# Kernel optimization log

Hardware: AMD Instinct MI355X
Metric: run time of the kernel (lower is better)

Reference implementation:

```python
import jax, jax.numpy as jnp
import numpy as np

B, S, D = 8, 2048, 2048  # seq_len must equal dim for this module's math to type-check


def setup_inputs() -> dict:
    key = jax.random.key(0)
    ks = jax.random.split(key, 9)
    sc = 1.0 / np.sqrt(D)
    return {
        "query": jax.random.normal(ks[0], (B, S, D), jnp.float32),
        "key_": jax.random.normal(ks[1], (B, S, D), jnp.float32),
        "value": jax.random.normal(ks[2], (B, S, D), jnp.float32),
        "Wq": jax.random.normal(ks[3], (D, D), jnp.float32) * sc,
        "bq": jax.random.normal(ks[4], (D,), jnp.float32) * 0.01,
        "Wk": jax.random.normal(ks[5], (D, D), jnp.float32) * sc,
        "bk": jax.random.normal(ks[6], (D,), jnp.float32) * 0.01,
        "Wv": jax.random.normal(ks[7], (D, D), jnp.float32) * sc,
        "bv": jax.random.normal(ks[8], (D,), jnp.float32) * 0.01,
    }


def reference(query, key_, value, Wq, bq, Wk, bk, Wv, bv):
    scale_factor = 1.0  # forward default
    # Linear projections (torch Linear: x @ W^T + b)
    q = jnp.einsum('bsd,ed->bse', query, Wq) + bq   # [B,S,D]
    k = jnp.einsum('bsd,ed->bse', key_, Wk) + bk    # [B,S,D]
    v = jnp.einsum('bsd,ed->bse', value, Wv) + bv   # [B,S,D]
    # Transpose last two dims, then matmul: [B,D,S] @ [B,D,S] (valid since S == D)
    qT = jnp.swapaxes(q, -2, -1)
    kT = jnp.swapaxes(k, -2, -1)
    qk = jnp.matmul(qT, kT) * scale_factor          # [B,D,S]
    attn = jax.nn.softmax(qk, axis=-1)
    # dropout_p = 0 -> identity
    out = jnp.matmul(attn, v)                       # [B,D,D]
    return jnp.swapaxes(out, -2, -1)
```

## Files before the change

kernel.cpp:

```cpp
#include <hip/hip_runtime.h>
#include <hip/hip_fp16.h>


using half8_t = __attribute__((ext_vector_type(8))) _Float16;
using f32x4   = __attribute__((ext_vector_type(4))) float;

static constexpr int NB = 8;
static constexpr int Sd = 2048;
static constexpr long MAT = (long)Sd * Sd;

__device__ __forceinline__ void gload16(const _Float16* g, _Float16* l) {
  __builtin_amdgcn_global_load_lds(
      (const __attribute__((address_space(1))) void*)g,
      (__attribute__((address_space(3))) void*)l, 16, 0, 0);
}
__device__ __forceinline__ void barrier_() { asm volatile("s_barrier" ::: "memory"); }
#define VMCNT(n) asm volatile("s_waitcnt vmcnt(" #n ")" ::: "memory")
#define SCHEDB() __builtin_amdgcn_sched_barrier(0)

template<bool SPLIT>
__global__ __launch_bounds__(256) void presplit(const float* __restrict__ in,
    _Float16* __restrict__ h, _Float16* __restrict__ l, long n8, float scl)
{
  long i = (long)blockIdx.x * 256 + threadIdx.x;
  const long stride = (long)gridDim.x * 256;
  for (; i < n8; i += stride) {
    const f32x4* p = (const f32x4*)(in + i * 8);
    f32x4 a = p[0], b = p[1];
    half8_t hh, ll;
#pragma unroll
    for (int j = 0; j < 4; j++) {
      float x = a[j] * scl; _Float16 hv = (_Float16)x;
      hh[j] = hv; if constexpr (SPLIT) ll[j] = (_Float16)(x - (float)hv);
      float y = b[j] * scl; _Float16 hw = (_Float16)y;
      hh[4 + j] = hw; if constexpr (SPLIT) ll[4 + j] = (_Float16)(y - (float)hw);
    }
    *(half8_t*)(h + i * 8) = hh;
    if constexpr (SPLIT) *(half8_t*)(l + i * 8) = ll;
  }
}

template<int NSEG, int BIAS, int OUT>
__global__ __launch_bounds__(512, 2) void gemm10(
    const _Float16* __restrict__ Ah, const _Float16* __restrict__ Al, long sA,
    const _Float16* __restrict__ Bh, long sB,
    const float* __restrict__ bias, float cscale,
    void* __restrict__ Cp, void* __restrict__ Clp, long sC)
{
  constexpr int NT = NSEG * 32;
  __shared__ __align__(16) _Float16 LA[4][8192];
  __shared__ __align__(16) _Float16 LB[4][8192];

  const int t = threadIdx.x, w = t >> 6, l = t & 63;

  const int wg = blockIdx.x;
  const int swz = (wg & 7) * 64 + (wg >> 3);
  const int bz = swz >> 6, rem = swz & 63;
  const int by = rem >> 3, bx = rem & 7;

  const _Float16* PAh = Ah + (size_t)bz * sA + (size_t)(by * 256) * Sd;
  const _Float16* PBh = Bh + (size_t)bz * sB + (size_t)(bx * 256) * Sd;
  const _Float16* PAl = (NSEG == 2)
      ? Al + (size_t)bz * sA + (size_t)(by * 256) * Sd : PAh;

  const int s7 = t & 7;
  const int lkS = (s7 >> 1) ^ ((t >> 3) & 3);
  const size_t srcoff = (size_t)(2 * (t >> 3) + (s7 & 1)) * Sd + lkS * 8;
  const int du0 = w * 512;

  const int wm = (w >> 2) * 128, wn = (w & 3) * 64;
  const int lm = l & 15, lkr = l >> 4;
  const int sprime = ((lkr ^ ((lm >> 1) & 3)) << 1) | (lm & 1);
  const int aoff = (wm >> 1) * 128 + (lm >> 1) * 128 + sprime * 16;
  const int boff = (wn >> 1) * 128 + (lm >> 1) * 128 + sprime * 16;

  auto srcA = [&](int hp) -> const _Float16* {
    if constexpr (NSEG == 2) return (hp >> 6) ? PAl : PAh;
    return PAh;
  };
  auto koOf = [&](int hp) -> int {
    if constexpr (NSEG == 2) return (hp & 63) * 32;
    return hp * 32;
  };
  auto stageH = [&](int hp) {
    const int u = hp & 3;
    const _Float16* a = srcA(hp) + koOf(hp);
    const _Float16* b = PBh + koOf(hp);
    gload16(a + srcoff, LA[u] + du0);
    gload16(a + srcoff + (size_t)128 * Sd, LA[u] + du0 + 4096);
    gload16(b + srcoff, LB[u] + du0);
    gload16(b + srcoff + (size_t)128 * Sd, LB[u] + du0 + 4096);
  };

  f32x4 acc[8][4] = {};
  half8_t fA0[8], fB0[4], fA1[8], fB1[4];

  auto readF = [&](int u, half8_t (&fa)[8], half8_t (&fb)[4]) {
#pragma unroll
    for (int f = 0; f < 8; f++)
      fa[f] = *(const half8_t*)((const char*)LA[u] + aoff + f * 1024);
#pragma unroll
    for (int n = 0; n < 4; n++)
      fb[n] = *(const half8_t*)((const char*)LB[u] + boff + n * 1024);
  };
  auto mfma32 = [&](const half8_t (&fa)[8], const half8_t (&fb)[4]) {
    __builtin_amdgcn_s_setprio(1);
#pragma unroll
    for (int f = 0; f < 8; f++)
#pragma unroll
      for (int n = 0; n < 4; n++)
        acc[f][n] = __builtin_amdgcn_mfma_f32_16x16x32_f16(fa[f], fb[n], acc[f][n], 0, 0, 0);
    __builtin_amdgcn_s_setprio(0);
  };

  stageH(0); stageH(1); stageH(2);
  VMCNT(4);
  barrier_();
  readF(0, fA0, fB0);

  for (int j = 0; j < NT - 1; ++j) {
    const int p0 = 2 * j;
    readF((p0 + 1) & 3, fA1, fB1);
    stageH(p0 + 3);
    SCHEDB();
    mfma32(fA0, fB0);
    VMCNT(4);
    barrier_();
    readF((p0 + 2) & 3, fA0, fB0);
    if (j < NT - 2) stageH(p0 + 4);
    SCHEDB();
    mfma32(fA1, fB1);
    if (j == NT - 2) { VMCNT(0); } else { VMCNT(4); }
    barrier_();
  }
  {
    const int p0 = 2 * (NT - 1);
    readF((p0 + 1) & 3, fA1, fB1);
    SCHEDB();
    mfma32(fA0, fB0);
    SCHEDB();
    mfma32(fA1, fB1);
  }

  const int row_base = by * 256 + wm + (lkr << 2);
  const int col_base = bx * 256 + wn + lm;
#pragma unroll
  for (int fm = 0; fm < 8; fm++)
#pragma unroll
    for (int fn = 0; fn < 4; fn++) {
      const int n = col_base + fn * 16;
      float bcol = 0.f;
      if constexpr (BIAS == 1) bcol = bias[n];
#pragma unroll
      for (int r = 0; r < 4; r++) {
        const int m = row_base + fm * 16 + r;
        float v = acc[fm][fn][r] * cscale;
        if constexpr (BIAS == 1) v += bcol;
        if constexpr (BIAS == 2) v += bias[m];
        const size_t ci = (size_t)bz * sC + (size_t)m * Sd + n;
        if constexpr (OUT == 0) ((float*)Cp)[ci] = v;
        else if constexpr (OUT == 1) ((_Float16*)Cp)[ci] = (_Float16)v;
        else if constexpr (OUT == 3) ((_Float16*)Cp)[ci] = (_Float16)(v * 16.0f);
        else {
          float sv = v * 16.0f;
          _Float16 hv = (_Float16)sv;
          ((_Float16*)Cp)[ci]  = hv;
          ((_Float16*)Clp)[ci] = (_Float16)(sv - (float)hv);
        }
      }
    }
}

__global__ __launch_bounds__(256) void softmax_rows(const float* __restrict__ X,
                                                    _Float16* __restrict__ P)
{
  __shared__ float red[4];
  const size_t row = blockIdx.x;
  const float* x = X + row * Sd;
  _Float16* p = P + row * Sd;
  const int t = threadIdx.x;
  float v[8];
  float mx = -1e30f;
#pragma unroll
  for (int i = 0; i < 8; i++) { v[i] = x[t + 256 * i]; mx = fmaxf(mx, v[i]); }
#pragma unroll
  for (int o = 32; o > 0; o >>= 1) mx = fmaxf(mx, __shfl_xor(mx, o, 64));
  if ((t & 63) == 0) red[t >> 6] = mx;
  __syncthreads();
  mx = fmaxf(fmaxf(red[0], red[1]), fmaxf(red[2], red[3]));
  __syncthreads();
  float s = 0.f;
#pragma unroll
  for (int i = 0; i < 8; i++) { v[i] = __expf(v[i] - mx); s += v[i]; }
#pragma unroll
  for (int o = 32; o > 0; o >>= 1) s += __shfl_xor(s, o, 64);
  if ((t & 63) == 0) red[t >> 6] = s;
  __syncthreads();
  s = red[0] + red[1] + red[2] + red[3];
  float inv = 1.f / s;
#pragma unroll
  for (int i = 0; i < 8; i++) p[t + 256 * i] = (_Float16)(v[i] * inv);
}

extern "C" void kernel_launch(void* const* d_in, const int* in_sizes, int n_in,
                              void* d_out, int out_size, void* d_ws, size_t ws_size,
                              hipStream_t stream)
{
  const float* query = (const float*)d_in[0];
  const float* key_  = (const float*)d_in[1];
  const float* value = (const float*)d_in[2];
  const float* Wq = (const float*)d_in[3];
  const float* bq = (const float*)d_in[4];
  const float* Wk = (const float*)d_in[5];
  const float* bk = (const float*)d_in[6];
  const float* Wv = (const float*)d_in[7];
  const float* bv = (const float*)d_in[8];

  char* ws = (char*)d_ws;
  char* ob = (char*)d_out;
  const size_t M64 = (size_t)NB * MAT * 2;

  _Float16* q_h  = (_Float16*)(ws);
  _Float16* k_h  = (_Float16*)(ws);
  _Float16* k_l  = (_Float16*)(ws + M64);
  float*    qk   = (float*)(ws);
  _Float16* qT_h = (_Float16*)(ws + 2 * M64);
  _Float16* qT_l = (_Float16*)(ws + 3 * M64);
  _Float16* P    = qT_h;
  _Float16* vT   = qT_l;
  _Float16* kk_h = (_Float16*)(ws + 4 * M64);
  _Float16* val_h = (_Float16*)(ws + 5 * M64);

  _Float16* wq_h = (_Float16*)(ob);
  _Float16* wq_l = (_Float16*)(ob + (MAT * 2));
  _Float16* wk_h = (_Float16*)(ob + 2 * (MAT * 2));
  _Float16* wv_h = (_Float16*)(ob + 3 * (MAT * 2));
  float* out = (float*)d_out;

  dim3 blk256(256), blk512(512);
  dim3 gg(512);
  const long NQ8 = (long)NB * MAT / 8;
  const long NW8 = MAT / 8;

  presplit<false><<<dim3(2048), blk256, 0, stream>>>(query, q_h, nullptr, NQ8, 16.f);
  presplit<true><<<dim3(2048), blk256, 0, stream>>>(Wq, wq_h, wq_l, NW8, 16.f);
  gemm10<2, 2, 2><<<gg, blk512, 0, stream>>>(wq_h, wq_l, 0, q_h, MAT,
                                             bq, 1.f / 256.f, qT_h, qT_l, MAT);
  presplit<true><<<dim3(2048), blk256, 0, stream>>>(key_, k_h, k_l, NQ8, 16.f);
  presplit<false><<<dim3(2048), blk256, 0, stream>>>(Wk, wk_h, nullptr, NW8, 16.f);
  gemm10<2, 1, 3><<<gg, blk512, 0, stream>>>(k_h, k_l, MAT, wk_h, 0,
                                             bk, 1.f / 256.f, kk_h, nullptr, MAT);
  gemm10<2, 0, 0><<<gg, blk512, 0, stream>>>(qT_h, qT_l, MAT, kk_h, MAT,
                                             nullptr, 1.f / 256.f, qk, nullptr, MAT);
  softmax_rows<<<dim3(NB * Sd), blk256, 0, stream>>>(qk, P);
  presplit<false><<<dim3(2048), blk256, 0, stream>>>(value, val_h, nullptr, NQ8, 1.f);
  presplit<false><<<dim3(2048), blk256, 0, stream>>>(Wv, wv_h, nullptr, NW8, 1.f);
  gemm10<1, 2, 1><<<gg, blk512, 0, stream>>>(wv_h, nullptr, 0, val_h, MAT,
                                             bv, 1.f, vT, nullptr, MAT);
  gemm10<1, 0, 0><<<gg, blk512, 0, stream>>>(vT, nullptr, MAT, P, MAT,
                                             nullptr, 1.f, out, nullptr, MAT);
}
```

Before: 1.168 ms.

## Load B fragments directly from global and reuse them across hi/lo A segments

The GEMM no longer stages the B operand through LDS. Each wave loads its B fragments straight from global memory into registers, and only A goes through the 4-slot LDS ring. In the split-precision case the hi and lo A chunks are interleaved so one B fragment load serves both MFMA passes, which halves B traffic. This cuts LDS footprint and LDS write/read work, but B reads now go per-wave from global or L2 with less coalescing and more redundancy across waves, and the wait counts change with the new pipeline.

```diff
diff --git a/kernel.cpp b/kernel.cpp
--- a/kernel.cpp
+++ b/kernel.cpp
@@ -41,15 +41,13 @@
 }
 
 template<int NSEG, int BIAS, int OUT>
-__global__ __launch_bounds__(512, 2) void gemm10(
+__global__ __launch_bounds__(512, 2) void gemm15(
     const _Float16* __restrict__ Ah, const _Float16* __restrict__ Al, long sA,
     const _Float16* __restrict__ Bh, long sB,
     const float* __restrict__ bias, float cscale,
     void* __restrict__ Cp, void* __restrict__ Clp, long sC)
 {
-  constexpr int NT = NSEG * 32;
   __shared__ __align__(16) _Float16 LA[4][8192];
-  __shared__ __align__(16) _Float16 LB[4][8192];
 
   const int t = threadIdx.x, w = t >> 6, l = t & 63;
 
@@ -72,36 +70,33 @@
   const int lm = l & 15, lkr = l >> 4;
   const int sprime = ((lkr ^ ((lm >> 1) & 3)) << 1) | (lm & 1);
   const int aoff = (wm >> 1) * 128 + (lm >> 1) * 128 + sprime * 16;
-  const int boff = (wn >> 1) * 128 + (lm >> 1) * 128 + sprime * 16;
-
-  auto srcA = [&](int hp) -> const _Float16* {
-    if constexpr (NSEG == 2) return (hp >> 6) ? PAl : PAh;
-    return PAh;
-  };
-  auto koOf = [&](int hp) -> int {
-    if constexpr (NSEG == 2) return (hp & 63) * 32;
-    return hp * 32;
-  };
-  auto stageH = [&](int hp) {
-    const int u = hp & 3;
-    const _Float16* a = srcA(hp) + koOf(hp);
-    const _Float16* b = PBh + koOf(hp);
-    gload16(a + srcoff, LA[u] + du0);
-    gload16(a + srcoff + (size_t)128 * Sd, LA[u] + du0 + 4096);
-    gload16(b + srcoff, LB[u] + du0);
-    gload16(b + srcoff + (size_t)128 * Sd, LB[u] + du0 + 4096);
+
+  const _Float16* pB = PBh + (size_t)(wn + lm) * Sd + lkr * 8;
+
+  auto stageA = [&](int p) {
+    const int slot = p & 3;
+    const _Float16* base;
+    if constexpr (NSEG == 2)
+      base = ((p & 1) ? PAl : PAh) + (p >> 1) * 32;
+    else
+      base = PAh + p * 32;
+    gload16(base + srcoff, LA[slot] + du0);
+    gload16(base + srcoff + (size_t)128 * Sd, LA[slot] + du0 + 4096);
   };
 
   f32x4 acc[8][4] = {};
-  half8_t fA0[8], fB0[4], fA1[8], fB1[4];
-
-  auto readF = [&](int u, half8_t (&fa)[8], half8_t (&fb)[4]) {
+  half8_t a0[8], a1[8], b0[4], b1[4];
+
+  auto readA = [&](int slot, half8_t (&fa)[8]) {
 #pragma unroll
     for (int f = 0; f < 8; f++)
-      fa[f] = *(const half8_t*)((const char*)LA[u] + aoff + f * 1024);
+      fa[f] = *(const half8_t*)((const char*)LA[slot] + aoff + f * 1024);
+  };
+  auto loadB = [&](int k, half8_t (&fb)[4]) {
+    const _Float16* base = pB + k * 32;
 #pragma unroll
     for (int n = 0; n < 4; n++)
-      fb[n] = *(const half8_t*)((const char*)LB[u] + boff + n * 1024);
+      fb[n] = *(const half8_t*)(base + (size_t)(n * 16) * Sd);
   };
   auto mfma32 = [&](const half8_t (&fa)[8], const half8_t (&fb)[4]) {
     __builtin_amdgcn_s_setprio(1);
@@ -113,33 +108,65 @@
     __builtin_amdgcn_s_setprio(0);
   };
 
-  stageH(0); stageH(1); stageH(2);
-  VMCNT(4);
-  barrier_();
-  readF(0, fA0, fB0);
-
-  for (int j = 0; j < NT - 1; ++j) {
-    const int p0 = 2 * j;
-    readF((p0 + 1) & 3, fA1, fB1);
-    stageH(p0 + 3);
-    SCHEDB();
-    mfma32(fA0, fB0);
-    VMCNT(4);
+  if constexpr (NSEG == 2) {
+    stageA(0); stageA(1); stageA(2);
+    loadB(0, b0);
+    VMCNT(6);
     barrier_();
-    readF((p0 + 2) & 3, fA0, fB0);
-    if (j < NT - 2) stageH(p0 + 4);
-    SCHEDB();
-    mfma32(fA1, fB1);
-    if (j == NT - 2) { VMCNT(0); } else { VMCNT(4); }
+    readA(0, a0);
+
+#define UNIT15(K, BC, BN)                                                 \
+    {                                                                     \
+      const int k_ = (K);                                                 \
+      const int pe = 2 * k_;                                              \
+                                     \
+      readA((pe + 1) & 3, a1);                                            \
+      if (pe <= 124) stageA(pe + 3);                                      \
+      if (k_ <= 62) loadB(k_ + 1, BN);                                    \
+      SCHEDB();                                                           \
+      mfma32(a0, BC);                                                     \
+      if (pe <= 124) { VMCNT(6); }                                        \
+      if (pe <= 125) barrier_();                                          \
+                                    \
+      if (pe + 2 <= 127) readA((pe + 2) & 3, a0);                         \
+      if (pe + 1 <= 124) stageA(pe + 4);                                  \
+      SCHEDB();                                                           \
+      mfma32(a1, BC);                                                     \
+      if (pe + 1 <= 124)      { VMCNT(6); }                               \
+      else if (pe + 1 == 125) { VMCNT(0); }                               \
+      if (pe + 1 <= 125) barrier_();                                      \
+    }
+
+    for (int kk = 0; kk < 32; ++kk) {
+      UNIT15(2 * kk,     b0, b1)
+      UNIT15(2 * kk + 1, b1, b0)
+    }
+#undef UNIT15
+  } else {
+    stageA(0); stageA(1); stageA(2);
+    loadB(0, b0);
+    VMCNT(6);
     barrier_();
-  }
-  {
-    const int p0 = 2 * (NT - 1);
-    readF((p0 + 1) & 3, fA1, fB1);
-    SCHEDB();
-    mfma32(fA0, fB0);
-    SCHEDB();
-    mfma32(fA1, fB1);
+    readA(0, a0);
+
+#define PH15(U, AC, AN, BC, BN)                                           \
+    {                                                                     \
+      const int u_ = (U);                                                 \
+      if (u_ <= 62) readA((u_ + 1) & 3, AN);                              \
+      if (u_ <= 60) stageA(u_ + 3);                                       \
+      if (u_ <= 62) loadB(u_ + 1, BN);                                    \
+      SCHEDB();                                                           \
+      mfma32(AC, BC);                                                     \
+      if (u_ <= 60)      { VMCNT(6); }                                    \
+      else if (u_ == 61) { VMCNT(0); }                                    \
+      if (u_ <= 62) barrier_();                                           \
+    }
+
+    for (int j = 0; j < 32; ++j) {
+      PH15(2 * j,     a0, a1, b0, b1)
+      PH15(2 * j + 1, a1, a0, b1, b0)
+    }
+#undef PH15
   }
 
   const int row_base = by * 256 + wm + (lkr << 2);
@@ -244,19 +271,19 @@
 
   presplit<false><<<dim3(2048), blk256, 0, stream>>>(query, q_h, nullptr, NQ8, 16.f);
   presplit<true><<<dim3(2048), blk256, 0, stream>>>(Wq, wq_h, wq_l, NW8, 16.f);
-  gemm10<2, 2, 2><<<gg, blk512, 0, stream>>>(wq_h, wq_l, 0, q_h, MAT,
+  gemm15<2, 2, 2><<<gg, blk512, 0, stream>>>(wq_h, wq_l, 0, q_h, MAT,
                                              bq, 1.f / 256.f, qT_h, qT_l, MAT);
   presplit<true><<<dim3(2048), blk256, 0, stream>>>(key_, k_h, k_l, NQ8, 16.f);
   presplit<false><<<dim3(2048), blk256, 0, stream>>>(Wk, wk_h, nullptr, NW8, 16.f);
-  gemm10<2, 1, 3><<<gg, blk512, 0, stream>>>(k_h, k_l, MAT, wk_h, 0,
+  gemm15<2, 1, 3><<<gg, blk512, 0, stream>>>(k_h, k_l, MAT, wk_h, 0,
                                              bk, 1.f / 256.f, kk_h, nullptr, MAT);
-  gemm10<2, 0, 0><<<gg, blk512, 0, stream>>>(qT_h, qT_l, MAT, kk_h, MAT,
+  gemm15<2, 0, 0><<<gg, blk512, 0, stream>>>(qT_h, qT_l, MAT, kk_h, MAT,
                                              nullptr, 1.f / 256.f, qk, nullptr, MAT);
   softmax_rows<<<dim3(NB * Sd), blk256, 0, stream>>>(qk, P);
   presplit<false><<<dim3(2048), blk256, 0, stream>>>(value, val_h, nullptr, NQ8, 1.f);
   presplit<false><<<dim3(2048), blk256, 0, stream>>>(Wv, wv_h, nullptr, NW8, 1.f);
-  gemm10<1, 2, 1><<<gg, blk512, 0, stream>>>(wv_h, nullptr, 0, val_h, MAT,
+  gemm15<1, 2, 1><<<gg, blk512, 0, stream>>>(wv_h, nullptr, 0, val_h, MAT,
                                              bv, 1.f, vT, nullptr, MAT);
-  gemm10<1, 0, 0><<<gg, blk512, 0, stream>>>(vT, nullptr, MAT, P, MAT,
+  gemm15<1, 0, 0><<<gg, blk512, 0, stream>>>(vT, nullptr, MAT, P, MAT,
                                              nullptr, 1.f, out, nullptr, MAT);
 }
```

After: 1.385 ms. 1.19x slower.
